# Kernel optimization log

Hardware: AMD Instinct MI355X
Metric: run time of the kernel (lower is better)

The kernel has to match this reference:

```python
import jax, jax.numpy as jnp
import numpy as np

DIM = 1024
HEADS = 16
HEAD_DIM = DIM // HEADS
B, T = 2, 2048


def setup_inputs() -> dict:
    key = jax.random.key(0)
    ks = jax.random.split(key, 6)
    x = jax.random.normal(ks[0], (B, T, DIM), dtype=jnp.float32)
    # Linear weights stored as [in, out] for x @ W + b
    w_qkv = jax.random.normal(ks[1], (DIM, 3 * DIM), dtype=jnp.float32) * (1.0 / np.sqrt(DIM))
    b_qkv = jnp.zeros((3 * DIM,), dtype=jnp.float32)
    w_out = jax.random.normal(ks[2], (DIM, DIM), dtype=jnp.float32) * (1.0 / np.sqrt(DIM))
    b_out = jnp.zeros((DIM,), dtype=jnp.float32)
    pos_bias = jax.random.normal(ks[3], (1, HEADS, 1, HEAD_DIM), dtype=jnp.float32) * 0.1
    return {"x": x, "w_qkv": w_qkv, "b_qkv": b_qkv, "w_out": w_out, "b_out": b_out, "pos_bias": pos_bias}


def reference(x, w_qkv, b_qkv, w_out, b_out, pos_bias):
    b, t, c = x.shape
    scale = HEAD_DIM ** -0.5
    qkv = x @ w_qkv + b_qkv                       # [B, T, 3C]
    q, k, v = jnp.split(qkv, 3, axis=-1)
    # [B, T, C] -> [B, H, T, Dh]
    def to_heads(z):
        return z.reshape(b, t, HEADS, HEAD_DIM).transpose(0, 2, 1, 3)
    q = to_heads(q) + pos_bias                    # learned query positional bias
    k = to_heads(k)
    v = to_heads(v)
    attn = jnp.einsum('bhqd,bhkd->bhqk', q, k) * scale
    causal = jnp.tril(jnp.ones((t, t), dtype=bool))
    attn = jnp.where(causal[None, None], attn, -jnp.inf)
    attn = jax.nn.softmax(attn, axis=-1)
    out = jnp.einsum('bhqk,bhkd->bhqd', attn, v)  # [B, H, T, Dh]
    out = out.transpose(0, 2, 1, 3).reshape(b, t, c)
    # dropout inactive (eval mode)
    return out @ w_out + b_out
```

## Files before the change

### kernel.cpp

```cpp
#include <hip/hip_runtime.h>

#define DIM 1024
#define HEADS 16
#define HD 64
#define BATCH 2
#define SEQ 2048
#define MROWS (BATCH*SEQ)
#define NQKV (3*DIM)
#define BK 32
#define NT (DIM/BK)
#define ALDT 72

typedef unsigned short u16;
typedef __attribute__((ext_vector_type(8))) short short8;
typedef __attribute__((ext_vector_type(4))) float f32x4;

#define QSCALE 0.1803368801111204f
#define DTHR 11.5f

__device__ __forceinline__ u16 f2bf(float f) {
  unsigned u = __float_as_uint(f);
  u += 0x7FFFu + ((u >> 16) & 1u);
  return (u16)(u >> 16);
}

__device__ __forceinline__ void gload16(const u16* g, u16* l) {
  __builtin_amdgcn_global_load_lds((const __attribute__((address_space(1))) unsigned int*)g,
                                   (__attribute__((address_space(3))) unsigned int*)l, 16, 0, 0);
}

__global__ void k_f32_to_bf16(const float* __restrict__ in, u16* __restrict__ out, int n8) {
  int i = blockIdx.x * blockDim.x + threadIdx.x;
  if (i >= n8) return;
  const float4* p = (const float4*)in + (size_t)i * 2;
  float4 a = p[0], b = p[1];
  short8 v;
  v[0] = (short)f2bf(a.x); v[1] = (short)f2bf(a.y);
  v[2] = (short)f2bf(a.z); v[3] = (short)f2bf(a.w);
  v[4] = (short)f2bf(b.x); v[5] = (short)f2bf(b.y);
  v[6] = (short)f2bf(b.z); v[7] = (short)f2bf(b.w);
  ((short8*)out)[i] = v;
}

__global__ void k_transpose2(const float* __restrict__ wqkv, u16* __restrict__ oqkv,
                             const float* __restrict__ wout, u16* __restrict__ oout) {
  __shared__ float tile[32][33];
  const int bx = blockIdx.x;
  const float* in; u16* out; int C, c0;
  if (bx < 96) { in = wqkv; out = oqkv; C = NQKV; c0 = bx * 32; }
  else         { in = wout; out = oout; C = DIM;  c0 = (bx - 96) * 32; }
  const int r0 = blockIdx.y * 32;
  const int tx = threadIdx.x, ty = threadIdx.y;
#pragma unroll
  for (int i = 0; i < 4; ++i)
    tile[ty + 8 * i][tx] = in[(size_t)(r0 + ty + 8 * i) * C + c0 + tx];
  __syncthreads();
#pragma unroll
  for (int i = 0; i < 4; ++i)
    out[(size_t)(c0 + ty + 8 * i) * DIM + r0 + tx] = f2bf(tile[tx][ty + 8 * i]);
}

#define GEMM_PREAMBLE(Aptr, Bptr)                                              \
  __shared__ u16 lds_[3 * 8192];                                               \
  const int tid = threadIdx.x;                                                 \
  const int lane = tid & 63;                                                   \
  const int wid = tid >> 6;                                                    \
  const int wm = wid >> 1, wn = wid & 1;                                       \
  const int rowA0 = blockIdx.y * 128;                                          \
  const int rowB0 = blockIdx.x * 128;                                          \
  const int rl = lane & 15, lg = lane >> 4;                                    \
  const int csw = (rl >> 1) & 3;                                               \
  const f32x4 fz = {0.f, 0.f, 0.f, 0.f};                                       \
  f32x4 acc[4][4];                                                             \
  _Pragma("unroll") for (int i = 0; i < 4; ++i)                                \
  _Pragma("unroll") for (int j = 0; j < 4; ++j) acc[i][j] = fz;                \
  const int srow = tid >> 2;                                                   \
  const int scol = ((tid & 3) ^ ((tid >> 3) & 3)) * 8;                         \
  const u16* gA = (Aptr) + (size_t)(rowA0 + srow) * DIM + scol;                \
  const u16* gB = (Bptr) + (size_t)(rowB0 + srow) * DIM + scol;                \
  auto stage = [&](int t, int j) {                                             \
    u16* d = lds_ + j * 8192;                                                  \
    gload16(gA + t * BK, d + tid * 8);                                         \
    gload16(gA + (size_t)64 * DIM + t * BK, d + 2048 + tid * 8);               \
    gload16(gB + t * BK, d + 4096 + tid * 8);                                  \
    gload16(gB + (size_t)64 * DIM + t * BK, d + 6144 + tid * 8);               \
  };                                                                           \
  auto compute = [&](int j) {                                                  \
    const u16* bufA = lds_ + j * 8192;                                         \
    const u16* bufB = bufA + 4096;                                             \
    short8 af[4], bfr[4];                                                      \
    _Pragma("unroll") for (int mf = 0; mf < 4; ++mf)                           \
      af[mf] = *(const short8*)(bufA + (wm * 64 + mf * 16 + rl) * 32 +         \
                                ((lg ^ csw) * 8));                             \
    _Pragma("unroll") for (int nf = 0; nf < 4; ++nf)                           \
      bfr[nf] = *(const short8*)(bufB + (wn * 64 + nf * 16 + rl) * 32 +        \
                                 ((lg ^ csw) * 8));                            \
    __builtin_amdgcn_s_setprio(1);                                             \
    _Pragma("unroll") for (int mf = 0; mf < 4; ++mf)                           \
    _Pragma("unroll") for (int nf = 0; nf < 4; ++nf)                           \
      acc[mf][nf] =                                                            \
          __builtin_amdgcn_mfma_f32_16x16x32_bf16(af[mf], bfr[nf],             \
                                                  acc[mf][nf], 0, 0, 0);       \
    __builtin_amdgcn_s_setprio(0);                                             \
  };                                                                           \
  stage(0, 0);                                                                 \
  stage(1, 1);                                                                 \
  asm volatile("s_waitcnt vmcnt(4)" ::: "memory");                             \
  __builtin_amdgcn_s_barrier();                                                \
  int cur = 0;                                                                 \
  _Pragma("unroll 3") for (int t = 0; t < NT - 2; ++t) {                       \
    int nb = cur + 2; if (nb >= 3) nb -= 3;                                    \
    stage(t + 2, nb);                                                          \
    compute(cur);                                                              \
    asm volatile("s_waitcnt vmcnt(4)" ::: "memory");                           \
    __builtin_amdgcn_s_barrier();                                              \
    cur = cur + 1; if (cur == 3) cur = 0;                                      \
  }                                                                            \
  compute(cur);                                                                \
  asm volatile("s_waitcnt vmcnt(0)" ::: "memory");                             \
  __builtin_amdgcn_s_barrier();                                                \
  cur = cur + 1; if (cur == 3) cur = 0;                                        \
  compute(cur);

__global__ __launch_bounds__(256) void k_gemm_qkv(
    const u16* __restrict__ A, const u16* __restrict__ Bt,
    const float* __restrict__ bias, const float* __restrict__ posb,
    u16* __restrict__ qb, u16* __restrict__ kb, u16* __restrict__ vtb) {
  GEMM_PREAMBLE(A, Bt)

#pragma unroll
  for (int mf = 0; mf < 4; ++mf) {
#pragma unroll
    for (int nf = 0; nf < 4; ++nf) {
#pragma unroll
      for (int r = 0; r < 4; ++r) {
        const int row = rowA0 + wm * 64 + mf * 16 + lg * 4 + r;
        const int col = rowB0 + wn * 64 + nf * 16 + rl;
        float v = acc[mf][nf][r] + bias[col];
        const int which = col >> 10;
        const int within = col & 1023;
        const int h = within >> 6, d = within & 63;
        const int bb = row >> 11, t = row & 2047;
        const size_t bh = (size_t)(bb * HEADS + h);
        if (which == 0) {
          v = (v + posb[within]) * QSCALE;
          qb[(bh * SEQ + t) * HD + d] = f2bf(v);
        } else if (which == 1) {
          kb[(bh * SEQ + t) * HD + d] = f2bf(v);
        } else {
          vtb[(bh * HD + d) * SEQ + t] = f2bf(v);
        }
      }
    }
  }
}

__global__ __launch_bounds__(256) void k_gemm_out(
    const u16* __restrict__ A, const u16* __restrict__ Bt,
    const float* __restrict__ bias, float* __restrict__ out) {
  __shared__ u16 lds_[3 * 6144];
  const int tid = threadIdx.x;
  const int lane = tid & 63;
  const int wid = tid >> 6;
  const int wm = wid >> 1, wn = wid & 1;
  const int rowA0 = blockIdx.y * 128;
  const int rowB0 = blockIdx.x * 64;
  const int rl = lane & 15, lg = lane >> 4;
  const int csw = (rl >> 1) & 3;
  const f32x4 fz = {0.f, 0.f, 0.f, 0.f};
  f32x4 acc[4][2];
#pragma unroll
  for (int i = 0; i < 4; ++i)
#pragma unroll
    for (int j = 0; j < 2; ++j) acc[i][j] = fz;
  const int srow = tid >> 2;
  const int scol = ((tid & 3) ^ ((tid >> 3) & 3)) * 8;
  const u16* gA = A + (size_t)(rowA0 + srow) * DIM + scol;
  const u16* gB = Bt + (size_t)(rowB0 + srow) * DIM + scol;
  auto stage = [&](int t, int j) {
    u16* d = lds_ + j * 6144;
    gload16(gA + t * BK, d + tid * 8);
    gload16(gA + (size_t)64 * DIM + t * BK, d + 2048 + tid * 8);
    gload16(gB + t * BK, d + 4096 + tid * 8);
  };
  auto compute = [&](int j) {
    const u16* bufA = lds_ + j * 6144;
    const u16* bufB = bufA + 4096;
    short8 af[4], bfr[2];
#pragma unroll
    for (int mf = 0; mf < 4; ++mf)
      af[mf] = *(const short8*)(bufA + (wm * 64 + mf * 16 + rl) * 32 + ((lg ^ csw) * 8));
#pragma unroll
    for (int nf = 0; nf < 2; ++nf)
      bfr[nf] = *(const short8*)(bufB + (wn * 32 + nf * 16 + rl) * 32 + ((lg ^ csw) * 8));
    __builtin_amdgcn_s_setprio(1);
#pragma unroll
    for (int mf = 0; mf < 4; ++mf)
#pragma unroll
      for (int nf = 0; nf < 2; ++nf)
        acc[mf][nf] = __builtin_amdgcn_mfma_f32_16x16x32_bf16(af[mf], bfr[nf], acc[mf][nf], 0, 0, 0);
    __builtin_amdgcn_s_setprio(0);
  };
  stage(0, 0);
  stage(1, 1);
  asm volatile("s_waitcnt vmcnt(3)" ::: "memory");
  __builtin_amdgcn_s_barrier();
  int cur = 0;
#pragma unroll 3
  for (int t = 0; t < NT - 2; ++t) {
    int nb = cur + 2; if (nb >= 3) nb -= 3;
    stage(t + 2, nb);
    compute(cur);
    asm volatile("s_waitcnt vmcnt(3)" ::: "memory");
    __builtin_amdgcn_s_barrier();
    cur = cur + 1; if (cur == 3) cur = 0;
  }
  compute(cur);
  asm volatile("s_waitcnt vmcnt(0)" ::: "memory");
  __builtin_amdgcn_s_barrier();
  cur = cur + 1; if (cur == 3) cur = 0;
  compute(cur);

#pragma unroll
  for (int mf = 0; mf < 4; ++mf)
#pragma unroll
    for (int nf = 0; nf < 2; ++nf)
#pragma unroll
      for (int r = 0; r < 4; ++r) {
        const int row = rowA0 + wm * 64 + mf * 16 + lg * 4 + r;
        const int col = rowB0 + wn * 32 + nf * 16 + rl;
        out[(size_t)row * DIM + col] = acc[mf][nf][r] + bias[col];
      }
}

__global__ __launch_bounds__(256) void k_attn(
    const u16* __restrict__ qg, const u16* __restrict__ kg, const u16* __restrict__ vg,
    u16* __restrict__ og) {
  __shared__ u16 lK[64 * ALDT];
  __shared__ u16 lV[64 * ALDT];
  const int tid = threadIdx.x;
  const int lane = tid & 63;
  const int wid = tid >> 6;
  const int rl = lane & 15, lg = lane >> 4;
  const int bh = blockIdx.x & 31;
  const int pair = blockIdx.x >> 5;
  const int b = bh >> 4, h = bh & 15;

  const u16* gK = kg + (size_t)bh * SEQ * HD;
  const u16* gV = vg + (size_t)bh * HD * SEQ;
  const int sr = tid >> 3;
  const int sc = (tid & 7) * 8;
  const int sl0 = (((2 * lg) & 3) << 4) + rl;
  const int sl1 = (((2 * lg + 1) & 3) << 4) + rl;
  const bool hi = (lg >= 2);

#pragma unroll 1
  for (int half = 0; half < 2; ++half) {
    const int qt = half ? pair : (31 - pair);
    const int qrow = qt * 64 + wid * 16 + rl;
    const u16* qptr = qg + ((size_t)bh * SEQ + qrow) * HD + lg * 8;
    const short8 aq0 = *(const short8*)(qptr);
    const short8 aq1 = *(const short8*)(qptr + 32);

    const f32x4 fz = {0.f, 0.f, 0.f, 0.f};
    f32x4 o[4];
#pragma unroll
    for (int dt = 0; dt < 4; ++dt) o[dt] = fz;
    float m = -1e30f, l = 0.f;

    int4 rka = *(const int4*)(gK + (size_t)sr * HD + sc);
    int4 rkb = *(const int4*)(gK + (size_t)(sr + 32) * HD + sc);
    int4 rva = *(const int4*)(gV + (size_t)sr * SEQ + sc);
    int4 rvb = *(const int4*)(gV + (size_t)(sr + 32) * SEQ + sc);

    for (int kt = 0; kt <= qt; ++kt) {
      __syncthreads();
      *(int4*)(lK + sr * ALDT + sc) = rka;
      *(int4*)(lK + (sr + 32) * ALDT + sc) = rkb;
      *(int4*)(lV + sr * ALDT + sc) = rva;
      *(int4*)(lV + (sr + 32) * ALDT + sc) = rvb;
      __syncthreads();
      if (kt < qt) {
        const int kv1 = (kt + 1) * 64;
        rka = *(const int4*)(gK + (size_t)(kv1 + sr) * HD + sc);
        rkb = *(const int4*)(gK + (size_t)(kv1 + sr + 32) * HD + sc);
        rva = *(const int4*)(gV + (size_t)sr * SEQ + kv1 + sc);
        rvb = *(const int4*)(gV + (size_t)(sr + 32) * SEQ + kv1 + sc);
      }

      f32x4 s[4];
#pragma unroll
      for (int ct = 0; ct < 4; ++ct) s[ct] = fz;
      __builtin_amdgcn_s_setprio(1);
#pragma unroll
      for (int ct = 0; ct < 4; ++ct) {
        short8 ak0 = *(const short8*)(lK + (ct * 16 + rl) * ALDT + lg * 8);
        short8 ak1 = *(const short8*)(lK + (ct * 16 + rl) * ALDT + 32 + lg * 8);
        s[ct] = __builtin_amdgcn_mfma_f32_16x16x32_bf16(ak0, aq0, s[ct], 0, 0, 0);
        s[ct] = __builtin_amdgcn_mfma_f32_16x16x32_bf16(ak1, aq1, s[ct], 0, 0, 0);
      }
      __builtin_amdgcn_s_setprio(0);

      if (kt == qt) {
#pragma unroll
        for (int ct = 0; ct < 4; ++ct)
#pragma unroll
          for (int r = 0; r < 4; ++r)
            if (kt * 64 + ct * 16 + lg * 4 + r > qrow) s[ct][r] = -1e30f;
      }

      float cm[4];
#pragma unroll
      for (int ct = 0; ct < 4; ++ct)
        cm[ct] = fmaxf(fmaxf(s[ct][0], s[ct][1]), fmaxf(s[ct][2], s[ct][3]));
      float pmax = fmaxf(fmaxf(cm[0], cm[1]), fmaxf(cm[2], cm[3]));
      pmax = fmaxf(pmax, __shfl_xor(pmax, 16, 64));
      pmax = fmaxf(pmax, __shfl_xor(pmax, 32, 64));

      if (__any(pmax - m > DTHR)) {
        const float mn = fmaxf(m, pmax);
        const float alpha = __builtin_amdgcn_exp2f(m - mn);
        m = mn;
        l *= alpha;
#pragma unroll
        for (int dt = 0; dt < 4; ++dt)
#pragma unroll
          for (int r = 0; r < 4; ++r) o[dt][r] *= alpha;
      }

      float rc[4];
      unsigned pk[4][2];
#pragma unroll
      for (int ct = 0; ct < 4; ++ct) {
        float p0 = __builtin_amdgcn_exp2f(s[ct][0] - m);
        float p1 = __builtin_amdgcn_exp2f(s[ct][1] - m);
        float p2 = __builtin_amdgcn_exp2f(s[ct][2] - m);
        float p3 = __builtin_amdgcn_exp2f(s[ct][3] - m);
        rc[ct] = (p0 + p1) + (p2 + p3);
        pk[ct][0] = (unsigned)f2bf(p0) | ((unsigned)f2bf(p1) << 16);
        pk[ct][1] = (unsigned)f2bf(p2) | ((unsigned)f2bf(p3) << 16);
      }
      l += (rc[0] + rc[1]) + (rc[2] + rc[3]);

#pragma unroll
      for (int kb2 = 0; kb2 < 2; ++kb2) {
        unsigned a0 = (unsigned)__shfl((int)pk[2 * kb2 + 0][0], sl0, 64);
        unsigned b0 = (unsigned)__shfl((int)pk[2 * kb2 + 1][0], sl0, 64);
        unsigned a1 = (unsigned)__shfl((int)pk[2 * kb2 + 0][1], sl0, 64);
        unsigned b1 = (unsigned)__shfl((int)pk[2 * kb2 + 1][1], sl0, 64);
        unsigned a2 = (unsigned)__shfl((int)pk[2 * kb2 + 0][0], sl1, 64);
        unsigned b2 = (unsigned)__shfl((int)pk[2 * kb2 + 1][0], sl1, 64);
        unsigned a3 = (unsigned)__shfl((int)pk[2 * kb2 + 0][1], sl1, 64);
        unsigned b3 = (unsigned)__shfl((int)pk[2 * kb2 + 1][1], sl1, 64);
        union { unsigned u[4]; short8 s8; } pu;
        pu.u[0] = hi ? b0 : a0;
        pu.u[1] = hi ? b1 : a1;
        pu.u[2] = hi ? b2 : a2;
        pu.u[3] = hi ? b3 : a3;
        __builtin_amdgcn_s_setprio(1);
#pragma unroll
        for (int dt = 0; dt < 4; ++dt) {
          short8 av = *(const short8*)(lV + (dt * 16 + rl) * ALDT + kb2 * 32 + lg * 8);
          o[dt] = __builtin_amdgcn_mfma_f32_16x16x32_bf16(av, pu.s8, o[dt], 0, 0, 0);
        }
        __builtin_amdgcn_s_setprio(0);
      }
    }

    l += __shfl_xor(l, 16, 64);
    l += __shfl_xor(l, 32, 64);
    const float linv = __builtin_amdgcn_rcpf(l);
    const size_t obase = ((size_t)b * SEQ + qrow) * DIM + h * HD;
#pragma unroll
    for (int dt = 0; dt < 4; ++dt) {
      union { u16 e[4]; uint2 v; } w;
      w.e[0] = f2bf(o[dt][0] * linv);
      w.e[1] = f2bf(o[dt][1] * linv);
      w.e[2] = f2bf(o[dt][2] * linv);
      w.e[3] = f2bf(o[dt][3] * linv);
      *(uint2*)(og + obase + dt * 16 + lg * 4) = w.v;
    }
  }
}

extern "C" void kernel_launch(void* const* d_in, const int* in_sizes, int n_in,
                              void* d_out, int out_size, void* d_ws, size_t ws_size,
                              hipStream_t stream) {
  const float* x = (const float*)d_in[0];
  const float* w_qkv = (const float*)d_in[1];
  const float* b_qkv = (const float*)d_in[2];
  const float* w_out = (const float*)d_in[3];
  const float* b_out = (const float*)d_in[4];
  const float* pos_bias = (const float*)d_in[5];
  float* out = (float*)d_out;

  u16* ws = (u16*)d_ws;
  u16* xb = ws;
  u16* wqkvb = xb + (size_t)MROWS * DIM;
  u16* woutb = wqkvb + (size_t)NQKV * DIM;
  u16* qb = woutb + (size_t)DIM * DIM;
  u16* kbuf = qb + (size_t)BATCH * HEADS * SEQ * HD;
  u16* vtb = kbuf + (size_t)BATCH * HEADS * SEQ * HD;
  u16* attnb = xb;

  k_f32_to_bf16<<<(MROWS * DIM / 8 + 255) / 256, 256, 0, stream>>>(x, xb, MROWS * DIM / 8);
  k_transpose2<<<dim3(128, DIM / 32), dim3(32, 8), 0, stream>>>(w_qkv, wqkvb, w_out, woutb);
  k_gemm_qkv<<<dim3(NQKV / 128, MROWS / 128), 256, 0, stream>>>(xb, wqkvb, b_qkv, pos_bias, qb, kbuf, vtb);
  k_attn<<<dim3(BATCH * HEADS * 16), 256, 0, stream>>>(qb, kbuf, vtb, attnb);
  k_gemm_out<<<dim3(DIM / 64, MROWS / 128), 256, 0, stream>>>(attnb, woutb, b_out, out);
}
```

Measured before the change: 203.3 us.

## Double-buffer attention K/V in LDS and route P through LDS

The attention kernel now keeps two LDS buffers for K/V tiles. The next tile is stored into the spare buffer while the current one is consumed, so each iteration needs one barrier instead of two. The softmax probabilities are staged through a per-wave LDS scratch area instead of eight cross-lane shuffles plus selects to build the MFMA operand. The manual bf16 rounding is replaced by the hardware v_cvt_pk_bf16_f32 pack instruction. LDS use per block rises from about 18KB to about 46KB, which may lower occupancy, and the P path adds LDS write/read latency.

```diff
diff --git a/kernel.cpp b/kernel.cpp
--- a/kernel.cpp
+++ b/kernel.cpp
@@ -22,6 +22,12 @@
   unsigned u = __float_as_uint(f);
   u += 0x7FFFu + ((u >> 16) & 1u);
   return (u16)(u >> 16);
+}
+
+__device__ __forceinline__ unsigned cvtpk(float lo, float hi) {
+  unsigned r;
+  asm("v_cvt_pk_bf16_f32 %0, %1, %2" : "=v"(r) : "v"(lo), "v"(hi));
+  return r;
 }
 
 __device__ __forceinline__ void gload16(const u16* g, u16* l) {
@@ -236,8 +242,9 @@
 __global__ __launch_bounds__(256) void k_attn(
     const u16* __restrict__ qg, const u16* __restrict__ kg, const u16* __restrict__ vg,
     u16* __restrict__ og) {
-  __shared__ u16 lK[64 * ALDT];
-  __shared__ u16 lV[64 * ALDT];
+  __shared__ u16 lK[2][64 * ALDT];
+  __shared__ u16 lV[2][64 * ALDT];
+  __shared__ u16 lP[4 * 16 * ALDT];
   const int tid = threadIdx.x;
   const int lane = tid & 63;
   const int wid = tid >> 6;
@@ -250,9 +257,7 @@
   const u16* gV = vg + (size_t)bh * HD * SEQ;
   const int sr = tid >> 3;
   const int sc = (tid & 7) * 8;
-  const int sl0 = (((2 * lg) & 3) << 4) + rl;
-  const int sl1 = (((2 * lg + 1) & 3) << 4) + rl;
-  const bool hi = (lg >= 2);
+  u16* pw = lP + wid * 16 * ALDT;
 
 #pragma unroll 1
   for (int half = 0; half < 2; ++half) {
@@ -272,21 +277,38 @@
     int4 rkb = *(const int4*)(gK + (size_t)(sr + 32) * HD + sc);
     int4 rva = *(const int4*)(gV + (size_t)sr * SEQ + sc);
     int4 rvb = *(const int4*)(gV + (size_t)(sr + 32) * SEQ + sc);
+    *(int4*)(lK[0] + sr * ALDT + sc) = rka;
+    *(int4*)(lK[0] + (sr + 32) * ALDT + sc) = rkb;
+    *(int4*)(lV[0] + sr * ALDT + sc) = rva;
+    *(int4*)(lV[0] + (sr + 32) * ALDT + sc) = rvb;
+    if (qt > 0) {
+      rka = *(const int4*)(gK + (size_t)(64 + sr) * HD + sc);
+      rkb = *(const int4*)(gK + (size_t)(64 + sr + 32) * HD + sc);
+      rva = *(const int4*)(gV + (size_t)sr * SEQ + 64 + sc);
+      rvb = *(const int4*)(gV + (size_t)(sr + 32) * SEQ + 64 + sc);
+    }
+    asm volatile("s_waitcnt lgkmcnt(0)" ::: "memory");
+    __builtin_amdgcn_s_barrier();
 
     for (int kt = 0; kt <= qt; ++kt) {
-      __syncthreads();
-      *(int4*)(lK + sr * ALDT + sc) = rka;
-      *(int4*)(lK + (sr + 32) * ALDT + sc) = rkb;
-      *(int4*)(lV + sr * ALDT + sc) = rva;
-      *(int4*)(lV + (sr + 32) * ALDT + sc) = rvb;
-      __syncthreads();
+      const int cur = kt & 1;
       if (kt < qt) {
-        const int kv1 = (kt + 1) * 64;
-        rka = *(const int4*)(gK + (size_t)(kv1 + sr) * HD + sc);
-        rkb = *(const int4*)(gK + (size_t)(kv1 + sr + 32) * HD + sc);
-        rva = *(const int4*)(gV + (size_t)sr * SEQ + kv1 + sc);
-        rvb = *(const int4*)(gV + (size_t)(sr + 32) * SEQ + kv1 + sc);
-      }
+        u16* dK = lK[cur ^ 1];
+        u16* dV = lV[cur ^ 1];
+        *(int4*)(dK + sr * ALDT + sc) = rka;
+        *(int4*)(dK + (sr + 32) * ALDT + sc) = rkb;
+        *(int4*)(dV + sr * ALDT + sc) = rva;
+        *(int4*)(dV + (sr + 32) * ALDT + sc) = rvb;
+        if (kt + 2 <= qt) {
+          const int kv2 = (kt + 2) * 64;
+          rka = *(const int4*)(gK + (size_t)(kv2 + sr) * HD + sc);
+          rkb = *(const int4*)(gK + (size_t)(kv2 + sr + 32) * HD + sc);
+          rva = *(const int4*)(gV + (size_t)sr * SEQ + kv2 + sc);
+          rvb = *(const int4*)(gV + (size_t)(sr + 32) * SEQ + kv2 + sc);
+        }
+      }
+      const u16* bK = lK[cur];
+      const u16* bV = lV[cur];
 
       f32x4 s[4];
 #pragma unroll
@@ -294,8 +316,8 @@
       __builtin_amdgcn_s_setprio(1);
 #pragma unroll
       for (int ct = 0; ct < 4; ++ct) {
-        short8 ak0 = *(const short8*)(lK + (ct * 16 + rl) * ALDT + lg * 8);
-        short8 ak1 = *(const short8*)(lK + (ct * 16 + rl) * ALDT + 32 + lg * 8);
+        short8 ak0 = *(const short8*)(bK + (ct * 16 + rl) * ALDT + lg * 8);
+        short8 ak1 = *(const short8*)(bK + (ct * 16 + rl) * ALDT + 32 + lg * 8);
         s[ct] = __builtin_amdgcn_mfma_f32_16x16x32_bf16(ak0, aq0, s[ct], 0, 0, 0);
         s[ct] = __builtin_amdgcn_mfma_f32_16x16x32_bf16(ak1, aq1, s[ct], 0, 0, 0);
       }
@@ -329,7 +351,6 @@
       }
 
       float rc[4];
-      unsigned pk[4][2];
 #pragma unroll
       for (int ct = 0; ct < 4; ++ct) {
         float p0 = __builtin_amdgcn_exp2f(s[ct][0] - m);
@@ -337,34 +358,27 @@
         float p2 = __builtin_amdgcn_exp2f(s[ct][2] - m);
         float p3 = __builtin_amdgcn_exp2f(s[ct][3] - m);
         rc[ct] = (p0 + p1) + (p2 + p3);
-        pk[ct][0] = (unsigned)f2bf(p0) | ((unsigned)f2bf(p1) << 16);
-        pk[ct][1] = (unsigned)f2bf(p2) | ((unsigned)f2bf(p3) << 16);
+        uint2 w;
+        w.x = cvtpk(p0, p1);
+        w.y = cvtpk(p2, p3);
+        *(uint2*)(pw + rl * ALDT + ct * 16 + lg * 4) = w;
       }
       l += (rc[0] + rc[1]) + (rc[2] + rc[3]);
 
 #pragma unroll
       for (int kb2 = 0; kb2 < 2; ++kb2) {
-        unsigned a0 = (unsigned)__shfl((int)pk[2 * kb2 + 0][0], sl0, 64);
-        unsigned b0 = (unsigned)__shfl((int)pk[2 * kb2 + 1][0], sl0, 64);
-        unsigned a1 = (unsigned)__shfl((int)pk[2 * kb2 + 0][1], sl0, 64);
-        unsigned b1 = (unsigned)__shfl((int)pk[2 * kb2 + 1][1], sl0, 64);
-        unsigned a2 = (unsigned)__shfl((int)pk[2 * kb2 + 0][0], sl1, 64);
-        unsigned b2 = (unsigned)__shfl((int)pk[2 * kb2 + 1][0], sl1, 64);
-        unsigned a3 = (unsigned)__shfl((int)pk[2 * kb2 + 0][1], sl1, 64);
-        unsigned b3 = (unsigned)__shfl((int)pk[2 * kb2 + 1][1], sl1, 64);
-        union { unsigned u[4]; short8 s8; } pu;
-        pu.u[0] = hi ? b0 : a0;
-        pu.u[1] = hi ? b1 : a1;
-        pu.u[2] = hi ? b2 : a2;
-        pu.u[3] = hi ? b3 : a3;
+        short8 pa = *(const short8*)(pw + rl * ALDT + kb2 * 32 + lg * 8);
         __builtin_amdgcn_s_setprio(1);
 #pragma unroll
         for (int dt = 0; dt < 4; ++dt) {
-          short8 av = *(const short8*)(lV + (dt * 16 + rl) * ALDT + kb2 * 32 + lg * 8);
-          o[dt] = __builtin_amdgcn_mfma_f32_16x16x32_bf16(av, pu.s8, o[dt], 0, 0, 0);
+          short8 av = *(const short8*)(bV + (dt * 16 + rl) * ALDT + kb2 * 32 + lg * 8);
+          o[dt] = __builtin_amdgcn_mfma_f32_16x16x32_bf16(av, pa, o[dt], 0, 0, 0);
         }
         __builtin_amdgcn_s_setprio(0);
       }
+
+      asm volatile("s_waitcnt lgkmcnt(0)" ::: "memory");
+      __builtin_amdgcn_s_barrier();
     }
 
     l += __shfl_xor(l, 16, 64);
@@ -373,12 +387,10 @@
     const size_t obase = ((size_t)b * SEQ + qrow) * DIM + h * HD;
 #pragma unroll
     for (int dt = 0; dt < 4; ++dt) {
-      union { u16 e[4]; uint2 v; } w;
-      w.e[0] = f2bf(o[dt][0] * linv);
-      w.e[1] = f2bf(o[dt][1] * linv);
-      w.e[2] = f2bf(o[dt][2] * linv);
-      w.e[3] = f2bf(o[dt][3] * linv);
-      *(uint2*)(og + obase + dt * 16 + lg * 4) = w.v;
+      uint2 w;
+      w.x = cvtpk(o[dt][0] * linv, o[dt][1] * linv);
+      w.y = cvtpk(o[dt][2] * linv, o[dt][3] * linv);
+      *(uint2*)(og + obase + dt * 16 + lg * 4) = w;
     }
   }
 }
```

Measured after the change: 196.8 us. 1.03x faster.
